# Kernel tuning notes

Measured on AMD Instinct MI355X. Metric: run time of the kernel, lower is better.

The kernel has to match this reference:

```python
import jax, jax.numpy as jnp
import numpy as np

B, C, H, S, DC = 32768, 1024, 1024, 8, 64  # batch, num_classes, hidden_dim, num_styles, calibrator dim

def setup_inputs() -> dict:
    key = jax.random.key(0)
    ks = jax.random.split(key, 12)
    inp = {
        "logits": jax.random.normal(ks[0], (B, C), dtype=jnp.float32),
        "style_idx": jax.random.randint(ks[1], (B,), 0, S, dtype=jnp.int32),
        # learned params
        "style_emb": jax.random.normal(ks[2], (S, H), dtype=jnp.float32),
        "Wa1": jax.random.normal(ks[3], (C + H, H), dtype=jnp.float32) * (1.0 / np.sqrt(C + H)),
        "ba1": jnp.zeros((H,), dtype=jnp.float32),
        "Wa2": jax.random.normal(ks[4], (H, C), dtype=jnp.float32) * (1.0 / np.sqrt(H)),
        "ba2": jnp.zeros((C,), dtype=jnp.float32),
        # per-style confidence calibrators: Linear(C,64) -> ReLU -> Linear(64,1) -> Sigmoid
        "Wc1": jax.random.normal(ks[5], (S, C, DC), dtype=jnp.float32) * (1.0 / np.sqrt(C)),
        "bc1": jnp.zeros((S, DC), dtype=jnp.float32),
        "Wc2": jax.random.normal(ks[6], (S, DC), dtype=jnp.float32) * (1.0 / np.sqrt(DC)),
        "bc2": jnp.zeros((S,), dtype=jnp.float32),
    }
    return inp

def reference(logits, style_idx, style_emb, Wa1, ba1, Wa2, ba2, Wc1, bc1, Wc2, bc2):
    # style embedding lookup + adapter MLP (residual on logits)
    emb = style_emb[style_idx]                                  # (B, H)
    combined = jnp.concatenate([logits, emb], axis=1)           # (B, C+H)
    hidden = jax.nn.relu(combined @ Wa1 + ba1)                  # (B, H)
    adjusted_logits = logits + hidden @ Wa2 + ba2               # (B, C)
    probs = jax.nn.softmax(adjusted_logits, axis=1)             # (B, C)
    # expert-routed confidence calibration: compute all styles densely, select per sample
    h = jax.nn.relu(jnp.einsum('bc,scd->bsd', probs, Wc1) + bc1)   # (B, S, DC)
    conf_all = jax.nn.sigmoid(jnp.einsum('bsd,sd->bs', h, Wc2) + bc2)  # (B, S)
    calibrated_confidence = jnp.take_along_axis(conf_all, style_idx[:, None].astype(jnp.int32), axis=1)  # (B, 1)
    return adjusted_logits, calibrated_confidence
```

## Files before the change

### kernel.cpp

```cpp
#include <hip/hip_runtime.h>
#include <hip/hip_bf16.h>
#include <stdint.h>

typedef __hip_bfloat16 bf16;
typedef __attribute__((ext_vector_type(8))) short short8;
typedef __attribute__((ext_vector_type(4))) float f32x4;

#define NB 32768
#define NC 1024
#define NH 1024
#define NS 8
#define NDC 64

__device__ __forceinline__ void gload_lds16(const void* g, void* l) {
    __builtin_amdgcn_global_load_lds((const __attribute__((address_space(1))) void*)g,
                                     (__attribute__((address_space(3))) void*)l, 16, 0, 0);
}

__device__ __forceinline__ short f2bf(float x) {
    bf16 h = __float2bfloat16(x);
    short s;
    __builtin_memcpy(&s, &h, 2);
    return s;
}

__global__ __launch_bounds__(256) void transpose_kernel(
    const float* __restrict__ in, bf16* __restrict__ out,
    int R, int Ccols, long long in_bs, long long out_bs)
{
    __shared__ float tile[32][33];
    const float* inb = in + (long long)blockIdx.z * in_bs;
    bf16* outb = out + (long long)blockIdx.z * out_bs;
    int c0 = blockIdx.x * 32, r0 = blockIdx.y * 32;
    int tx = threadIdx.x, ty = threadIdx.y;
#pragma unroll
    for (int i = 0; i < 32; i += 8)
        tile[ty + i][tx] = inb[(size_t)(r0 + ty + i) * Ccols + c0 + tx];
    __syncthreads();
#pragma unroll
    for (int i = 0; i < 32; i += 8)
        outb[(size_t)(c0 + ty + i) * R + r0 + tx] = __float2bfloat16(tile[tx][ty + i]);
}

__global__ __launch_bounds__(256) void style_partial_kernel(
    const float* __restrict__ style_emb, const float* __restrict__ Wa1,
    float* __restrict__ partial)
{
    const int h = (blockIdx.x & 3) * 256 + threadIdx.x;
    const int ks = blockIdx.x >> 2;
    float acc[NS];
#pragma unroll
    for (int s = 0; s < NS; ++s) acc[s] = 0.f;
#pragma unroll
    for (int kk = 0; kk < 16; ++kk) {
        const int k = ks * 16 + kk;
        const float w = Wa1[(size_t)(NC + k) * NH + h];
#pragma unroll
        for (int s = 0; s < NS; ++s)
            acc[s] += style_emb[s * NH + k] * w;
    }
#pragma unroll
    for (int s = 0; s < NS; ++s)
        partial[((size_t)ks * NS + s) * NH + h] = acc[s];
}

__global__ __launch_bounds__(256) void style_reduce_kernel(
    const float* __restrict__ partial, const float* __restrict__ ba1,
    float* __restrict__ out)
{
    const int i = blockIdx.x * 256 + threadIdx.x;
    const int h = i & (NH - 1);
    const int s = i >> 10;
    float acc = ba1[h];
#pragma unroll 8
    for (int ks = 0; ks < 64; ++ks)
        acc += partial[((size_t)ks * NS + s) * NH + h];
    out[i] = acc;
}

template<int MODE>
__global__ __launch_bounds__(256, 2) void gemm_kernel(
    const void* __restrict__ Ain, const bf16* __restrict__ BT,
    bf16* __restrict__ Cb, float* __restrict__ Cf,
    int N, int K,
    const float* __restrict__ style_contrib, const int* __restrict__ style_idx,
    const float* __restrict__ resid, const float* __restrict__ bias,
    const float* __restrict__ bc1, const float* __restrict__ Wc2,
    const float* __restrict__ bc2, float* __restrict__ conf_out)
{
    __shared__ short lA[128 * 64];
    __shared__ short lB[128 * 64];

    const int t = threadIdx.x;
    const int lane = t & 63;
    const int wave = t >> 6;
    const int wr = wave >> 1;
    const int wc = wave & 1;

    const int nwg = gridDim.x * gridDim.y;
    const int flat = blockIdx.y * gridDim.x + blockIdx.x;
    const int cpx = nwg >> 3;
    const int swz = (flat & 7) * cpx + (flat >> 3);
    const int bm0 = (swz / gridDim.x) * 128;
    const int bn0 = (swz % gridDim.x) * 128;

    const int r08 = t >> 3;
    const int clog = t & 7;
    const int csrc = clog ^ (r08 & 7);

    const int mrow = lane & 15;
    const int quad = lane >> 4;
    const int mrow7 = mrow & 7;

    f32x4 acc[4][4];
#pragma unroll
    for (int i = 0; i < 4; ++i)
#pragma unroll
        for (int j = 0; j < 4; ++j) acc[i][j] = (f32x4){0.f, 0.f, 0.f, 0.f};

    const float* gAf = (const float*)Ain + (size_t)(bm0 + r08) * K + clog * 8;
    const bf16*  gAb = (const bf16*)Ain + (size_t)(bm0 + r08) * K + csrc * 8;
    const bf16*  gB  = BT + (size_t)(bn0 + r08) * K + csrc * 8;

    for (int k0 = 0; k0 < K; k0 += 64) {
        if (MODE == 0) {
#pragma unroll
            for (int q = 0; q < 4; ++q) {
                const int row = q * 32 + r08;
                const float* src = gAf + (size_t)q * 32 * K + k0;
                float4 a = *(const float4*)(src);
                float4 b = *(const float4*)(src + 4);
                short8 v;
                v[0] = f2bf(a.x); v[1] = f2bf(a.y); v[2] = f2bf(a.z); v[3] = f2bf(a.w);
                v[4] = f2bf(b.x); v[5] = f2bf(b.y); v[6] = f2bf(b.z); v[7] = f2bf(b.w);
                *(short8*)(lA + row * 64 + (clog ^ (row & 7)) * 8) = v;
            }
        } else {
#pragma unroll
            for (int q = 0; q < 4; ++q)
                gload_lds16(gAb + (size_t)q * 32 * K + k0, lA + q * 2048 + t * 8);
        }
#pragma unroll
        for (int q = 0; q < 4; ++q)
            gload_lds16(gB + (size_t)q * 32 * K + k0, lB + q * 2048 + t * 8);

        __syncthreads();

#pragma unroll
        for (int kk = 0; kk < 2; ++kk) {
            const int coff = ((kk * 4 + quad) ^ mrow7) * 8;
            short8 af[4], bfr[4];
#pragma unroll
            for (int i = 0; i < 4; ++i)
                af[i] = *(const short8*)(lA + (wr * 64 + i * 16 + mrow) * 64 + coff);
#pragma unroll
            for (int j = 0; j < 4; ++j)
                bfr[j] = *(const short8*)(lB + (wc * 64 + j * 16 + mrow) * 64 + coff);
#pragma unroll
            for (int i = 0; i < 4; ++i)
#pragma unroll
                for (int j = 0; j < 4; ++j)
                    acc[i][j] = __builtin_amdgcn_mfma_f32_16x16x32_bf16(af[i], bfr[j], acc[i][j], 0, 0, 0);
        }

        __syncthreads();
    }

    if (MODE == 2) {
        const int s_w = (bn0 >> 6) + wc;
        float bcv[4], wcv[4];
#pragma unroll
        for (int j = 0; j < 4; ++j) {
            const int d = j * 16 + mrow;
            bcv[j] = bc1[s_w * NDC + d];
            wcv[j] = Wc2[s_w * NDC + d];
        }
        const float bias2 = bc2[s_w];
#pragma unroll
        for (int i = 0; i < 4; ++i) {
#pragma unroll
            for (int r = 0; r < 4; ++r) {
                const int grow = bm0 + wr * 64 + i * 16 + quad * 4 + r;
                float p = 0.f;
#pragma unroll
                for (int j = 0; j < 4; ++j)
                    p += fmaxf(acc[i][j][r] + bcv[j], 0.f) * wcv[j];
#pragma unroll
                for (int off = 1; off < 16; off <<= 1) p += __shfl_xor(p, off, 64);
                if (mrow == 0 && style_idx[grow] == s_w)
                    conf_out[grow] = 1.0f / (1.0f + __expf(-(p + bias2)));
            }
        }
        return;
    }

#pragma unroll
    for (int i = 0; i < 4; ++i) {
#pragma unroll
        for (int r = 0; r < 4; ++r) {
            const int grow = bm0 + wr * 64 + i * 16 + quad * 4 + r;
            const float* scrow = nullptr;
            const float* resrow = nullptr;
            if (MODE == 0) scrow = style_contrib + (size_t)style_idx[grow] * N;
            if (MODE == 1) resrow = resid + (size_t)grow * N;
#pragma unroll
            for (int j = 0; j < 4; ++j) {
                const int gcol = bn0 + wc * 64 + j * 16 + mrow;
                float v = acc[i][j][r];
                if (MODE == 0) {
                    v += scrow[gcol];
                    v = fmaxf(v, 0.f);
                    Cb[(size_t)grow * N + gcol] = __float2bfloat16(v);
                } else {
                    v += resrow[gcol] + bias[gcol];
                    Cf[(size_t)grow * N + gcol] = v;
                }
            }
        }
    }
}

__global__ __launch_bounds__(256) void softmax_kernel(
    const float* __restrict__ in, bf16* __restrict__ out)
{
    const size_t row = blockIdx.x;
    const float* x = in + row * NC;
    bf16* o = out + row * NC;
    const int t = threadIdx.x;
    __shared__ float red[8];

    float v[4];
    float m = -1e30f;
#pragma unroll
    for (int i = 0; i < 4; ++i) {
        v[i] = x[t + i * 256];
        m = fmaxf(m, v[i]);
    }
#pragma unroll
    for (int off = 1; off < 64; off <<= 1) m = fmaxf(m, __shfl_xor(m, off, 64));
    const int wv = t >> 6;
    if ((t & 63) == 0) red[wv] = m;
    __syncthreads();
    const float gm = fmaxf(fmaxf(red[0], red[1]), fmaxf(red[2], red[3]));

    float s = 0.f;
#pragma unroll
    for (int i = 0; i < 4; ++i) {
        v[i] = __expf(v[i] - gm);
        s += v[i];
    }
#pragma unroll
    for (int off = 1; off < 64; off <<= 1) s += __shfl_xor(s, off, 64);
    if ((t & 63) == 0) red[4 + wv] = s;
    __syncthreads();
    const float inv = 1.0f / (red[4] + red[5] + red[6] + red[7]);
#pragma unroll
    for (int i = 0; i < 4; ++i) o[t + i * 256] = __float2bfloat16(v[i] * inv);
}

extern "C" void kernel_launch(void* const* d_in, const int* in_sizes, int n_in,
                              void* d_out, int out_size, void* d_ws, size_t ws_size,
                              hipStream_t stream) {
    const float* logits    = (const float*)d_in[0];
    const int*   style_idx = (const int*)d_in[1];
    const float* style_emb = (const float*)d_in[2];
    const float* Wa1       = (const float*)d_in[3];
    const float* ba1       = (const float*)d_in[4];
    const float* Wa2       = (const float*)d_in[5];
    const float* ba2       = (const float*)d_in[6];
    const float* Wc1       = (const float*)d_in[7];
    const float* bc1       = (const float*)d_in[8];
    const float* Wc2       = (const float*)d_in[9];
    const float* bc2       = (const float*)d_in[10];

    char* ws = (char*)d_ws;
    bf16* hidden = (bf16*)ws;          ws += (size_t)NB * NH * 2;
    bf16* W1T = (bf16*)ws;             ws += (size_t)NC * NH * 2;
    bf16* W2T = (bf16*)ws;             ws += (size_t)NH * NC * 2;
    bf16* Wc1T = (bf16*)ws;            ws += (size_t)NS * NDC * NC * 2;
    float* style_contrib = (float*)ws; ws += (size_t)NS * NH * 4;
    float* style_partial = (float*)ws; ws += (size_t)64 * NS * NH * 4;

    float* adjusted = (float*)d_out;
    float* conf_out = (float*)d_out + (size_t)NB * NC;

    dim3 tb(32, 8);
    transpose_kernel<<<dim3(32, 32, 1), tb, 0, stream>>>(Wa1, W1T, NC, NH, 0, 0);
    transpose_kernel<<<dim3(32, 32, 1), tb, 0, stream>>>(Wa2, W2T, NH, NC, 0, 0);
    transpose_kernel<<<dim3(2, 32, NS), tb, 0, stream>>>(Wc1, Wc1T, NC, NDC,
                                                         (long long)NC * NDC, (long long)NDC * NC);
    style_partial_kernel<<<256, 256, 0, stream>>>(style_emb, Wa1, style_partial);
    style_reduce_kernel<<<NS * NH / 256, 256, 0, stream>>>(style_partial, ba1, style_contrib);

    gemm_kernel<0><<<dim3(NH / 128, NB / 128), 256, 0, stream>>>(
        logits, W1T, hidden, nullptr, NH, NC, style_contrib, style_idx, nullptr, nullptr,
        nullptr, nullptr, nullptr, nullptr);
    gemm_kernel<1><<<dim3(NC / 128, NB / 128), 256, 0, stream>>>(
        hidden, W2T, nullptr, adjusted, NC, NH, nullptr, nullptr, logits, ba2,
        nullptr, nullptr, nullptr, nullptr);
    softmax_kernel<<<NB, 256, 0, stream>>>(adjusted, hidden);
    gemm_kernel<2><<<dim3((NS * NDC) / 128, NB / 128), 256, 0, stream>>>(
        hidden, Wc1T, nullptr, nullptr, NS * NDC, NC, nullptr, style_idx, nullptr, nullptr,
        bc1, Wc2, bc2, conf_out);
}
```

Measured before the change: 498.8 us.

## Fuse softmax into calibrator GEMM, merge prep kernels, prefetch fp32 A tiles

Drops the separate softmax kernel. The calibrator GEMM now reads the fp32 adjusted logits, computes row max and sum-reciprocal per 128-row tile in a prologue, then applies exp and normalisation while converting A tiles to bf16. This removes a full bf16 probability write and read. The five prep launches (three transposes plus the two-stage style projection) become one kernel, with 4 blocks each looping over all 1024 k values. MODE 0 and MODE 2 also prefetch the next A tile into registers during compute. The costs are re-reading adjusted twice per N-tile (the grid has 4 N columns), redundant exp work, and a serial style-projection tail in the prep kernel.

```diff
diff --git a/kernel.cpp b/kernel.cpp
--- a/kernel.cpp
+++ b/kernel.cpp
@@ -24,58 +24,59 @@
     return s;
 }
 
-__global__ __launch_bounds__(256) void transpose_kernel(
-    const float* __restrict__ in, bf16* __restrict__ out,
-    int R, int Ccols, long long in_bs, long long out_bs)
+__global__ __launch_bounds__(256) void prep_kernel(
+    const float* __restrict__ Wa1, const float* __restrict__ Wa2,
+    const float* __restrict__ Wc1, const float* __restrict__ style_emb,
+    const float* __restrict__ ba1,
+    bf16* __restrict__ W1T, bf16* __restrict__ W2T, bf16* __restrict__ Wc1T,
+    float* __restrict__ style_contrib)
 {
     __shared__ float tile[32][33];
-    const float* inb = in + (long long)blockIdx.z * in_bs;
-    bf16* outb = out + (long long)blockIdx.z * out_bs;
-    int c0 = blockIdx.x * 32, r0 = blockIdx.y * 32;
-    int tx = threadIdx.x, ty = threadIdx.y;
-#pragma unroll
-    for (int i = 0; i < 32; i += 8)
-        tile[ty + i][tx] = inb[(size_t)(r0 + ty + i) * Ccols + c0 + tx];
-    __syncthreads();
-#pragma unroll
-    for (int i = 0; i < 32; i += 8)
-        outb[(size_t)(c0 + ty + i) * R + r0 + tx] = __float2bfloat16(tile[tx][ty + i]);
-}
-
-__global__ __launch_bounds__(256) void style_partial_kernel(
-    const float* __restrict__ style_emb, const float* __restrict__ Wa1,
-    float* __restrict__ partial)
-{
-    const int h = (blockIdx.x & 3) * 256 + threadIdx.x;
-    const int ks = blockIdx.x >> 2;
-    float acc[NS];
-#pragma unroll
-    for (int s = 0; s < NS; ++s) acc[s] = 0.f;
-#pragma unroll
-    for (int kk = 0; kk < 16; ++kk) {
-        const int k = ks * 16 + kk;
-        const float w = Wa1[(size_t)(NC + k) * NH + h];
+    const int b = blockIdx.x;
+    const int tx = threadIdx.x, ty = threadIdx.y;
+
+    if (b < 2560) {
+        const float* in; bf16* out; int R, Ccols, bx, by;
+        long long ioff = 0, ooff = 0;
+        if (b < 1024) {
+            in = Wa1; out = W1T; R = NC; Ccols = NH; bx = b & 31; by = b >> 5;
+        } else if (b < 2048) {
+            const int i = b - 1024;
+            in = Wa2; out = W2T; R = NH; Ccols = NC; bx = i & 31; by = i >> 5;
+        } else {
+            const int i = b - 2048;
+            const int bz = i >> 6, rem = i & 63;
+            by = rem >> 1; bx = rem & 1;
+            in = Wc1; out = Wc1T; R = NC; Ccols = NDC;
+            ioff = (long long)bz * NC * NDC; ooff = (long long)bz * NDC * NC;
+        }
+        const float* inb = in + ioff;
+        bf16* outb = out + ooff;
+        const int c0 = bx * 32, r0 = by * 32;
+#pragma unroll
+        for (int i = 0; i < 32; i += 8)
+            tile[ty + i][tx] = inb[(size_t)(r0 + ty + i) * Ccols + c0 + tx];
+        __syncthreads();
+#pragma unroll
+        for (int i = 0; i < 32; i += 8)
+            outb[(size_t)(c0 + ty + i) * R + r0 + tx] = __float2bfloat16(tile[tx][ty + i]);
+    } else {
+        const int t = ty * 32 + tx;
+        const int h = (b - 2560) * 256 + t;
+        float acc[NS];
+#pragma unroll
+        for (int s = 0; s < NS; ++s) acc[s] = 0.f;
+#pragma unroll 4
+        for (int k = 0; k < NH; ++k) {
+            const float w = Wa1[(size_t)(NC + k) * NH + h];
+#pragma unroll
+            for (int s = 0; s < NS; ++s)
+                acc[s] += style_emb[s * NH + k] * w;
+        }
 #pragma unroll
         for (int s = 0; s < NS; ++s)
-            acc[s] += style_emb[s * NH + k] * w;
-    }
-#pragma unroll
-    for (int s = 0; s < NS; ++s)
-        partial[((size_t)ks * NS + s) * NH + h] = acc[s];
-}
-
-__global__ __launch_bounds__(256) void style_reduce_kernel(
-    const float* __restrict__ partial, const float* __restrict__ ba1,
-    float* __restrict__ out)
-{
-    const int i = blockIdx.x * 256 + threadIdx.x;
-    const int h = i & (NH - 1);
-    const int s = i >> 10;
-    float acc = ba1[h];
-#pragma unroll 8
-    for (int ks = 0; ks < 64; ++ks)
-        acc += partial[((size_t)ks * NS + s) * NH + h];
-    out[i] = acc;
+            style_contrib[s * NH + h] = ba1[h] + acc[s];
+    }
 }
 
 template<int MODE>
@@ -90,6 +91,8 @@
 {
     __shared__ short lA[128 * 64];
     __shared__ short lB[128 * 64];
+    __shared__ float sm_m[128];
+    __shared__ float sm_is[128];
 
     const int t = threadIdx.x;
     const int lane = t & 63;
@@ -122,49 +125,122 @@
     const bf16*  gAb = (const bf16*)Ain + (size_t)(bm0 + r08) * K + csrc * 8;
     const bf16*  gB  = BT + (size_t)(bn0 + r08) * K + csrc * 8;
 
-    for (int k0 = 0; k0 < K; k0 += 64) {
-        if (MODE == 0) {
-#pragma unroll
-            for (int q = 0; q < 4; ++q) {
-                const int row = q * 32 + r08;
-                const float* src = gAf + (size_t)q * 32 * K + k0;
-                float4 a = *(const float4*)(src);
-                float4 b = *(const float4*)(src + 4);
-                short8 v;
-                v[0] = f2bf(a.x); v[1] = f2bf(a.y); v[2] = f2bf(a.z); v[3] = f2bf(a.w);
-                v[4] = f2bf(b.x); v[5] = f2bf(b.y); v[6] = f2bf(b.z); v[7] = f2bf(b.w);
-                *(short8*)(lA + row * 64 + (clog ^ (row & 7)) * 8) = v;
+    if (MODE == 2) {
+        for (int rr = 0; rr < 32; ++rr) {
+            const int row = wave * 32 + rr;
+            const float* x = (const float*)Ain + (size_t)(bm0 + row) * K + lane * 4;
+            float4 v0 = *(const float4*)(x);
+            float4 v1 = *(const float4*)(x + 256);
+            float4 v2 = *(const float4*)(x + 512);
+            float4 v3 = *(const float4*)(x + 768);
+            float m = fmaxf(fmaxf(fmaxf(v0.x, v0.y), fmaxf(v0.z, v0.w)),
+                            fmaxf(fmaxf(v1.x, v1.y), fmaxf(v1.z, v1.w)));
+            m = fmaxf(m, fmaxf(fmaxf(fmaxf(v2.x, v2.y), fmaxf(v2.z, v2.w)),
+                               fmaxf(fmaxf(v3.x, v3.y), fmaxf(v3.z, v3.w))));
+#pragma unroll
+            for (int off = 1; off < 64; off <<= 1) m = fmaxf(m, __shfl_xor(m, off, 64));
+            float s = __expf(v0.x - m) + __expf(v0.y - m) + __expf(v0.z - m) + __expf(v0.w - m)
+                    + __expf(v1.x - m) + __expf(v1.y - m) + __expf(v1.z - m) + __expf(v1.w - m)
+                    + __expf(v2.x - m) + __expf(v2.y - m) + __expf(v2.z - m) + __expf(v2.w - m)
+                    + __expf(v3.x - m) + __expf(v3.y - m) + __expf(v3.z - m) + __expf(v3.w - m);
+#pragma unroll
+            for (int off = 1; off < 64; off <<= 1) s += __shfl_xor(s, off, 64);
+            if (lane == 0) { sm_m[row] = m; sm_is[row] = 1.0f / s; }
+        }
+        __syncthreads();
+    }
+
+    const int NT = K >> 6;
+    float4 arA[4], arB[4];
+
+#define LOADA(kt)                                                              \
+    do {                                                                       \
+        _Pragma("unroll")                                                      \
+        for (int q = 0; q < 4; ++q) {                                          \
+            const float* src_ = gAf + (size_t)q * 32 * K + (kt) * 64;          \
+            arA[q] = *(const float4*)(src_);                                   \
+            arB[q] = *(const float4*)(src_ + 4);                               \
+        }                                                                      \
+    } while (0)
+
+#define WRITEA()                                                               \
+    do {                                                                       \
+        _Pragma("unroll")                                                      \
+        for (int q = 0; q < 4; ++q) {                                          \
+            const int row_ = q * 32 + r08;                                     \
+            float e0 = arA[q].x, e1 = arA[q].y, e2 = arA[q].z, e3 = arA[q].w;  \
+            float e4 = arB[q].x, e5 = arB[q].y, e6 = arB[q].z, e7 = arB[q].w;  \
+            if (MODE == 2) {                                                   \
+                const float m_ = sm_m[row_], is_ = sm_is[row_];                \
+                e0 = __expf(e0 - m_) * is_; e1 = __expf(e1 - m_) * is_;        \
+                e2 = __expf(e2 - m_) * is_; e3 = __expf(e3 - m_) * is_;        \
+                e4 = __expf(e4 - m_) * is_; e5 = __expf(e5 - m_) * is_;        \
+                e6 = __expf(e6 - m_) * is_; e7 = __expf(e7 - m_) * is_;        \
+            }                                                                  \
+            short8 v_;                                                         \
+            v_[0] = f2bf(e0); v_[1] = f2bf(e1); v_[2] = f2bf(e2); v_[3] = f2bf(e3); \
+            v_[4] = f2bf(e4); v_[5] = f2bf(e5); v_[6] = f2bf(e6); v_[7] = f2bf(e7); \
+            *(short8*)(lA + row_ * 64 + (clog ^ (r08 & 7)) * 8) = v_;          \
+        }                                                                      \
+    } while (0)
+
+#define STAGEB(kt)                                                             \
+    do {                                                                       \
+        _Pragma("unroll")                                                      \
+        for (int q = 0; q < 4; ++q)                                            \
+            gload_lds16(gB + (size_t)q * 32 * K + (kt) * 64, lB + q * 2048 + t * 8); \
+    } while (0)
+
+#define COMPUTE()                                                              \
+    do {                                                                       \
+        _Pragma("unroll")                                                      \
+        for (int kk = 0; kk < 2; ++kk) {                                       \
+            const int coff = ((kk * 4 + quad) ^ mrow7) * 8;                    \
+            short8 af[4], bfr[4];                                              \
+            _Pragma("unroll")                                                  \
+            for (int i = 0; i < 4; ++i)                                        \
+                af[i] = *(const short8*)(lA + (wr * 64 + i * 16 + mrow) * 64 + coff); \
+            _Pragma("unroll")                                                  \
+            for (int j = 0; j < 4; ++j)                                        \
+                bfr[j] = *(const short8*)(lB + (wc * 64 + j * 16 + mrow) * 64 + coff); \
+            _Pragma("unroll")                                                  \
+            for (int i = 0; i < 4; ++i)                                        \
+                _Pragma("unroll")                                              \
+                for (int j = 0; j < 4; ++j)                                    \
+                    acc[i][j] = __builtin_amdgcn_mfma_f32_16x16x32_bf16(af[i], bfr[j], acc[i][j], 0, 0, 0); \
+        }                                                                      \
+    } while (0)
+
+    if (MODE == 1) {
+        for (int kt = 0; kt < NT; ++kt) {
+#pragma unroll
+            for (int q = 0; q < 4; ++q)
+                gload_lds16(gAb + (size_t)q * 32 * K + kt * 64, lA + q * 2048 + t * 8);
+            STAGEB(kt);
+            __syncthreads();
+            COMPUTE();
+            __syncthreads();
+        }
+    } else {
+        LOADA(0);
+        WRITEA();
+        STAGEB(0);
+        __syncthreads();
+        for (int kt = 0; kt < NT; ++kt) {
+            if (kt + 1 < NT) LOADA(kt + 1);
+            COMPUTE();
+            if (kt + 1 < NT) {
+                __syncthreads();
+                WRITEA();
+                STAGEB(kt + 1);
+                __syncthreads();
             }
-        } else {
-#pragma unroll
-            for (int q = 0; q < 4; ++q)
-                gload_lds16(gAb + (size_t)q * 32 * K + k0, lA + q * 2048 + t * 8);
-        }
-#pragma unroll
-        for (int q = 0; q < 4; ++q)
-            gload_lds16(gB + (size_t)q * 32 * K + k0, lB + q * 2048 + t * 8);
-
-        __syncthreads();
-
-#pragma unroll
-        for (int kk = 0; kk < 2; ++kk) {
-            const int coff = ((kk * 4 + quad) ^ mrow7) * 8;
-            short8 af[4], bfr[4];
-#pragma unroll
-            for (int i = 0; i < 4; ++i)
-                af[i] = *(const short8*)(lA + (wr * 64 + i * 16 + mrow) * 64 + coff);
-#pragma unroll
-            for (int j = 0; j < 4; ++j)
-                bfr[j] = *(const short8*)(lB + (wc * 64 + j * 16 + mrow) * 64 + coff);
-#pragma unroll
-            for (int i = 0; i < 4; ++i)
-#pragma unroll
-                for (int j = 0; j < 4; ++j)
-                    acc[i][j] = __builtin_amdgcn_mfma_f32_16x16x32_bf16(af[i], bfr[j], acc[i][j], 0, 0, 0);
-        }
-
-        __syncthreads();
-    }
+        }
+    }
+#undef LOADA
+#undef WRITEA
+#undef STAGEB
+#undef COMPUTE
 
     if (MODE == 2) {
         const int s_w = (bn0 >> 6) + wc;
@@ -218,44 +294,6 @@
             }
         }
     }
-}
-
-__global__ __launch_bounds__(256) void softmax_kernel(
-    const float* __restrict__ in, bf16* __restrict__ out)
-{
-    const size_t row = blockIdx.x;
-    const float* x = in + row * NC;
-    bf16* o = out + row * NC;
-    const int t = threadIdx.x;
-    __shared__ float red[8];
-
-    float v[4];
-    float m = -1e30f;
-#pragma unroll
-    for (int i = 0; i < 4; ++i) {
-        v[i] = x[t + i * 256];
-        m = fmaxf(m, v[i]);
-    }
-#pragma unroll
-    for (int off = 1; off < 64; off <<= 1) m = fmaxf(m, __shfl_xor(m, off, 64));
-    const int wv = t >> 6;
-    if ((t & 63) == 0) red[wv] = m;
-    __syncthreads();
-    const float gm = fmaxf(fmaxf(red[0], red[1]), fmaxf(red[2], red[3]));
-
-    float s = 0.f;
-#pragma unroll
-    for (int i = 0; i < 4; ++i) {
-        v[i] = __expf(v[i] - gm);
-        s += v[i];
-    }
-#pragma unroll
-    for (int off = 1; off < 64; off <<= 1) s += __shfl_xor(s, off, 64);
-    if ((t & 63) == 0) red[4 + wv] = s;
-    __syncthreads();
-    const float inv = 1.0f / (red[4] + red[5] + red[6] + red[7]);
-#pragma unroll
-    for (int i = 0; i < 4; ++i) o[t + i * 256] = __float2bfloat16(v[i] * inv);
 }
 
 extern "C" void kernel_launch(void* const* d_in, const int* in_sizes, int n_in,
@@ -279,18 +317,12 @@
     bf16* W2T = (bf16*)ws;             ws += (size_t)NH * NC * 2;
     bf16* Wc1T = (bf16*)ws;            ws += (size_t)NS * NDC * NC * 2;
     float* style_contrib = (float*)ws; ws += (size_t)NS * NH * 4;
-    float* style_partial = (float*)ws; ws += (size_t)64 * NS * NH * 4;
 
     float* adjusted = (float*)d_out;
     float* conf_out = (float*)d_out + (size_t)NB * NC;
 
-    dim3 tb(32, 8);
-    transpose_kernel<<<dim3(32, 32, 1), tb, 0, stream>>>(Wa1, W1T, NC, NH, 0, 0);
-    transpose_kernel<<<dim3(32, 32, 1), tb, 0, stream>>>(Wa2, W2T, NH, NC, 0, 0);
-    transpose_kernel<<<dim3(2, 32, NS), tb, 0, stream>>>(Wc1, Wc1T, NC, NDC,
-                                                         (long long)NC * NDC, (long long)NDC * NC);
-    style_partial_kernel<<<256, 256, 0, stream>>>(style_emb, Wa1, style_partial);
-    style_reduce_kernel<<<NS * NH / 256, 256, 0, stream>>>(style_partial, ba1, style_contrib);
+    prep_kernel<<<2564, dim3(32, 8), 0, stream>>>(
+        Wa1, Wa2, Wc1, style_emb, ba1, W1T, W2T, Wc1T, style_contrib);
 
     gemm_kernel<0><<<dim3(NH / 128, NB / 128), 256, 0, stream>>>(
         logits, W1T, hidden, nullptr, NH, NC, style_contrib, style_idx, nullptr, nullptr,
@@ -298,8 +330,7 @@
     gemm_kernel<1><<<dim3(NC / 128, NB / 128), 256, 0, stream>>>(
         hidden, W2T, nullptr, adjusted, NC, NH, nullptr, nullptr, logits, ba2,
         nullptr, nullptr, nullptr, nullptr);
-    softmax_kernel<<<NB, 256, 0, stream>>>(adjusted, hidden);
     gemm_kernel<2><<<dim3((NS * NDC) / 128, NB / 128), 256, 0, stream>>>(
-        hidden, Wc1T, nullptr, nullptr, NS * NDC, NC, nullptr, style_idx, nullptr, nullptr,
+        adjusted, Wc1T, nullptr, nullptr, NS * NDC, NC, nullptr, style_idx, nullptr, nullptr,
         bc1, Wc2, bc2, conf_out);
 }
```

Result: slower. 699.2 us (+40.2%).
